# Optimization experiments

Measured on AMD Instinct MI355X. Metric: run time of the kernel, lower is better.

Reference implementation:

```python
import jax, jax.numpy as jnp
import numpy as np

EPS = 1e-6
NEG_SLOPE = 0.2

B, C_IN, N, K = 4, 64, 40960, 16
C_OUT = 64


def setup_inputs() -> dict:
    key = jax.random.key(0)
    k1, k2, k3 = jax.random.split(key, 3)
    feature = jax.random.normal(k1, (B, C_IN, N, 1), dtype=jnp.float32)
    neigh_idx = jax.random.randint(k2, (B, N, K), 0, N, dtype=jnp.int64)
    # 1x1 conv kernel [C_out, C_in] (kaiming-like scale), no bias since bn=True
    W = jax.random.normal(k3, (C_OUT, C_IN), dtype=jnp.float32) * np.float32(np.sqrt(2.0 / C_IN))
    gamma = jnp.ones((C_OUT,), dtype=jnp.float32)
    beta = jnp.zeros((C_OUT,), dtype=jnp.float32)
    return {"feature": feature, "W": W, "gamma": gamma, "beta": beta, "neigh_idx": neigh_idx}


def _gather_neighbour(pc, neigh_idx):
    # pc: [B, C, N]; neigh_idx: [B, N, K] -> [B, C, N, K]
    return jax.vmap(lambda p, idx: p[:, idx])(pc, neigh_idx)


def reference(feature, W, gamma, beta, neigh_idx):
    pc = feature[..., 0]                       # [B, C, N]
    f_neigh = _gather_neighbour(pc, neigh_idx) # [B, C, N, K]
    x = jnp.concatenate([feature, f_neigh], axis=-1)  # [B, C, N, K+1]
    # 1x1 conv (no bias)
    y = jnp.einsum('oc,bcnk->bonk', W, x)      # [B, C_out, N, K+1]
    # BatchNorm2d (training mode: batch stats over B,N,K+1), eps=1e-6
    mean = jnp.mean(y, axis=(0, 2, 3), keepdims=True)
    var = jnp.mean(jnp.square(y - mean), axis=(0, 2, 3), keepdims=True)
    yn = (y - mean) * jax.lax.rsqrt(var + EPS)
    yn = yn * gamma[None, :, None, None] + beta[None, :, None, None]
    # LeakyReLU(0.2)
    act = jnp.where(yn >= 0, yn, NEG_SLOPE * yn)
    # sum over neighbor axis, keepdim
    return jnp.sum(act, axis=-1, keepdims=True)  # [B, C_out, N, 1]
```

## Files before the change

kernel.cpp:

```cpp
#include <hip/hip_runtime.h>
#include <hip/hip_fp16.h>

typedef _Float16 h2 __attribute__((ext_vector_type(2)));
typedef _Float16 f16x8 __attribute__((ext_vector_type(8)));
typedef float f32x4 __attribute__((ext_vector_type(4)));
typedef unsigned int u32x4 __attribute__((ext_vector_type(4)));

#define BB 4
#define CIN 64
#define COUT 64
#define NN 40960
#define KK 16
#define GBLK (BB * NN / 256)
#define HP 32
#define HR 2
#define HBINS (NN / HR)
#define HWORDS (HBINS / 4)
#define GTP 72

__global__ __launch_bounds__(256) void k_hist(const int* __restrict__ idx,
                                              unsigned int* __restrict__ hist,
                                              float* __restrict__ sums) {
    __shared__ unsigned int bins[HWORDS];
    const int tid = threadIdx.x;
    const int p = blockIdx.x >> 3;
    const int b = (blockIdx.x & 7) >> 1;
    const int r = blockIdx.x & 1;
    const int lo = r * HBINS;

    if (blockIdx.x == 0 && tid < 128) sums[tid] = 0.f;

#pragma unroll
    for (int i = 0; i < HWORDS / 256; ++i) bins[i * 256 + tid] = 0u;
    __syncthreads();

    const int SHARE = NN * KK / HP;
    const int4* src = (const int4*)(idx + (size_t)b * NN * KK + (size_t)p * SHARE);
#pragma unroll 4
    for (int i = 0; i < SHARE / 4 / 256; ++i) {
        int4 v = src[i * 256 + tid];
        unsigned a0 = (unsigned)(v.x - lo), a1 = (unsigned)(v.y - lo);
        unsigned a2 = (unsigned)(v.z - lo), a3 = (unsigned)(v.w - lo);
        if (a0 < HBINS) atomicAdd(&bins[a0 >> 2], 1u << ((a0 & 3) * 8));
        if (a1 < HBINS) atomicAdd(&bins[a1 >> 2], 1u << ((a1 & 3) * 8));
        if (a2 < HBINS) atomicAdd(&bins[a2 >> 2], 1u << ((a2 & 3) * 8));
        if (a3 < HBINS) atomicAdd(&bins[a3 >> 2], 1u << ((a3 & 3) * 8));
    }
    __syncthreads();
    unsigned int* dst = hist + (size_t)((b * HP + p) * HR + r) * HWORDS;
#pragma unroll
    for (int i = 0; i < HWORDS / 256; ++i) dst[i * 256 + tid] = bins[i * 256 + tid];
}

__global__ __launch_bounds__(256) void k_gemm(const float* __restrict__ feat,
                                              const float* __restrict__ W,
                                              const unsigned int* __restrict__ hist,
                                              __half* __restrict__ g,
                                              float* __restrict__ sums) {
    __shared__ __half gt[4][64][GTP];
    __shared__ float  red[2][64][17];
    __shared__ float  w_s[256];

    const int tid   = threadIdx.x;
    const int b     = (blockIdx.x & 7) >> 1;
    const int chunk = (blockIdx.x & 1) * 80 + (blockIdx.x >> 3);
    const int n0    = chunk * 256;

    {
        const int n  = n0 + tid;
        const int r  = n / HBINS;
        const int ml = n - r * HBINS;
        const int w  = ml >> 2;
        const int sh = (ml & 3) * 8;
        unsigned s = 1u;
#pragma unroll
        for (int p = 0; p < HP; ++p)
            s += (hist[(size_t)((b * HP + p) * HR + r) * HWORDS + w] >> sh) & 0xffu;
        w_s[tid] = (float)s;
    }

    const int wv = tid >> 6;
    const int l  = tid & 63;
    const int lr = l & 15;
    const int lg = l >> 4;

    f16x8 bf[2][4];
#pragma unroll
    for (int ot = 0; ot < 4; ++ot)
#pragma unroll
        for (int kc = 0; kc < 2; ++kc) {
            const float* wp = W + (size_t)(ot * 16 + lr) * 64 + kc * 32 + lg * 8;
            float4 w0 = *(const float4*)(wp);
            float4 w1 = *(const float4*)(wp + 4);
            f16x8 t;
            t[0] = (_Float16)w0.x; t[1] = (_Float16)w0.y;
            t[2] = (_Float16)w0.z; t[3] = (_Float16)w0.w;
            t[4] = (_Float16)w1.x; t[5] = (_Float16)w1.y;
            t[6] = (_Float16)w1.z; t[7] = (_Float16)w1.w;
            bf[kc][ot] = t;
        }

    f32x4 acc[4][4];
#pragma unroll
    for (int i = 0; i < 4; ++i)
#pragma unroll
        for (int j = 0; j < 4; ++j) acc[i][j] = (f32x4)0.f;

    const float* fb = feat + (size_t)b * CIN * NN;
    const int nbase = n0 + wv * 64;

#pragma unroll
    for (int nt = 0; nt < 4; ++nt) {
        const int n = nbase + nt * 16 + lr;
#pragma unroll
        for (int kc = 0; kc < 2; ++kc) {
            const float* ap = fb + (size_t)(kc * 32 + lg * 8) * NN + n;
            f16x8 a;
#pragma unroll
            for (int j = 0; j < 8; ++j) a[j] = (_Float16)ap[(size_t)j * NN];
#pragma unroll
            for (int ot = 0; ot < 4; ++ot)
                acc[nt][ot] = __builtin_amdgcn_mfma_f32_16x16x32_f16(
                    a, bf[kc][ot], acc[nt][ot], 0, 0, 0);
        }
    }

    float wr[4][4];
#pragma unroll
    for (int nt = 0; nt < 4; ++nt)
#pragma unroll
        for (int r = 0; r < 4; ++r)
            wr[nt][r] = w_s[wv * 64 + nt * 16 + lg * 4 + r];

    float s1[4] = {0.f, 0.f, 0.f, 0.f}, s2[4] = {0.f, 0.f, 0.f, 0.f};
#pragma unroll
    for (int nt = 0; nt < 4; ++nt)
#pragma unroll
        for (int ot = 0; ot < 4; ++ot)
#pragma unroll
            for (int r = 0; r < 4; ++r) {
                float y = acc[nt][ot][r];
                float t = wr[nt][r] * y;
                s1[ot] += t;
                s2[ot] += t * y;
            }

#pragma unroll
    for (int nt = 0; nt < 4; ++nt)
#pragma unroll
        for (int ot = 0; ot < 4; ++ot)
#pragma unroll
            for (int r = 0; r < 4; ++r)
                gt[wv][nt * 16 + lg * 4 + r][ot * 16 + lr] = (__half)acc[nt][ot][r];

#pragma unroll
    for (int ot = 0; ot < 4; ++ot) {
        red[0][ot * 16 + lr][wv * 4 + lg] = s1[ot];
        red[1][ot * 16 + lr][wv * 4 + lg] = s2[ot];
    }
    __syncthreads();

    __half* gb = g + ((size_t)b * NN + n0) * 64;
#pragma unroll
    for (int i = 0; i < 8; ++i) {
        int nl = i * 32 + (tid >> 3);
        int o8 = (tid & 7) * 8;
        uint4 v = *(const uint4*)&gt[nl >> 6][nl & 63][o8];
        *(uint4*)&gb[(size_t)nl * 64 + o8] = v;
    }

    if (tid < 128) {
        int s = tid >> 6, o = tid & 63;
        float acc_s = 0.f;
#pragma unroll
        for (int t = 0; t < 16; ++t) acc_s += red[s][o][t];
        atomicAdd(&sums[s * 64 + o], acc_s);
    }
}

__global__ __launch_bounds__(256) void k_final(const __half* __restrict__ g,
                                               const int* __restrict__ idx,
                                               const float* __restrict__ sums,
                                               const float* __restrict__ gamma,
                                               const float* __restrict__ beta,
                                               float* __restrict__ out) {
    const int tid  = threadIdx.x;
    const int lane = tid & 63;
    const int wave = tid >> 6;
    const int b     = (blockIdx.x & 7) >> 1;
    const int chunk = ((blockIdx.x >> 3) << 1) | (blockIdx.x & 1);
    const int n0    = chunk * 64;

    __shared__ int   idx_s[64 * 17];
    __shared__ float tile[64 * 65];
    __shared__ float prm[128];

    {
        const u32x4* src = (const u32x4*)(idx + ((size_t)b * NN + n0) * KK);
        u32x4 v = __builtin_nontemporal_load(src + tid);
        int row = tid >> 2, col = (tid & 3) * 4;
        idx_s[row * 17 + col + 0] = (int)v.x;
        idx_s[row * 17 + col + 1] = (int)v.y;
        idx_s[row * 17 + col + 2] = (int)v.z;
        idx_s[row * 17 + col + 3] = (int)v.w;
    }

    if (tid < 64) {
        const double TOT = (double)BB * NN * (KK + 1);
        double mean = (double)sums[tid] / TOT;
        double var  = (double)sums[64 + tid] / TOT - mean * mean;
        double inv  = 1.0 / sqrt(var + 1e-6);
        float scale = (float)inv * gamma[tid];
        float shift = beta[tid] - (float)mean * scale;
        prm[tid]      = scale;
        prm[64 + tid] = shift;
    }
    __syncthreads();

    const int r  = lane >> 3;
    const int q8 = (lane & 7) * 8;
    h2 sc2[4], sh2[4];
#pragma unroll
    for (int h = 0; h < 4; ++h) {
        h2 a, s;
        a.x = (_Float16)prm[q8 + 2 * h];      a.y = (_Float16)prm[q8 + 2 * h + 1];
        s.x = (_Float16)prm[64 + q8 + 2 * h]; s.y = (_Float16)prm[64 + q8 + 2 * h + 1];
        sc2[h] = a; sh2[h] = s;
    }

    const __half* gb = g + (size_t)b * NN * 64;

#pragma unroll
    for (int rr = 0; rr < 2; ++rr) {
        const int nl = wave * 16 + rr * 8 + r;
        h2 acc[4];
#pragma unroll
        for (int h = 0; h < 4; ++h) acc[h] = (h2)(_Float16)0;

#pragma unroll
        for (int k = -1; k < KK; ++k) {
            int m = (k < 0) ? (n0 + nl) : idx_s[nl * 17 + k];
            union { uint4 u; h2 h[4]; } U;
            U.u = *(const uint4*)(gb + (size_t)m * 64 + q8);
#pragma unroll
            for (int h = 0; h < 4; ++h) {
                h2 t = U.h[h] * sc2[h] + sh2[h];
                acc[h] += __builtin_elementwise_max(t, t * (_Float16)0.2f);
            }
        }
        float* tr = &tile[nl * 65 + q8];
#pragma unroll
        for (int h = 0; h < 4; ++h) {
            tr[2 * h]     = (float)acc[h].x;
            tr[2 * h + 1] = (float)acc[h].y;
        }
    }
    __syncthreads();
    const int j   = tid & 63;
    const int sub = tid >> 6;
#pragma unroll
    for (int ob = 0; ob < 16; ++ob) {
        int o = ob * 4 + sub;
        __builtin_nontemporal_store(tile[j * 65 + o],
                                    &out[(size_t)(b * 64 + o) * NN + n0 + j]);
    }
}

extern "C" void kernel_launch(void* const* d_in, const int* in_sizes, int n_in,
                              void* d_out, int out_size, void* d_ws, size_t ws_size,
                              hipStream_t stream) {
    const float* feat  = (const float*)d_in[0];
    const float* W     = (const float*)d_in[1];
    const float* gamma = (const float*)d_in[2];
    const float* beta  = (const float*)d_in[3];
    const int*   idx   = (const int*)d_in[4];
    float* out = (float*)d_out;

    char* ws = (char*)d_ws;
    __half* g = (__half*)ws;
    size_t off = (size_t)BB * NN * 64 * sizeof(__half);
    unsigned int* hist = (unsigned int*)(ws + off);
    off += (size_t)BB * HP * HR * HWORDS * sizeof(unsigned int);
    float* sums = (float*)(ws + off);

    k_hist<<<BB * HP * HR, 256, 0, stream>>>(idx, hist, sums);
    k_gemm<<<GBLK, 256, 0, stream>>>(feat, W, hist, g, sums);
    k_final<<<(BB * NN) / 64, 256, 0, stream>>>(g, idx, sums, gamma, beta, out);
}
```

Before: 158.4 us.

## Swap MFMA operands to write g directly and reduce stats via shuffles

Measured after the change: 155.7 us, median of 2. Within noise of the previous version (-1.7%).

```diff
diff --git a/kernel.cpp b/kernel.cpp
--- a/kernel.cpp
+++ b/kernel.cpp
@@ -4,7 +4,6 @@
 typedef _Float16 h2 __attribute__((ext_vector_type(2)));
 typedef _Float16 f16x8 __attribute__((ext_vector_type(8)));
 typedef float f32x4 __attribute__((ext_vector_type(4)));
-typedef unsigned int u32x4 __attribute__((ext_vector_type(4)));
 
 #define BB 4
 #define CIN 64
@@ -16,7 +15,6 @@
 #define HR 2
 #define HBINS (NN / HR)
 #define HWORDS (HBINS / 4)
-#define GTP 72
 
 __global__ __launch_bounds__(256) void k_hist(const int* __restrict__ idx,
                                               unsigned int* __restrict__ hist,
@@ -57,9 +55,8 @@
                                               const unsigned int* __restrict__ hist,
                                               __half* __restrict__ g,
                                               float* __restrict__ sums) {
-    __shared__ __half gt[4][64][GTP];
-    __shared__ float  red[2][64][17];
-    __shared__ float  w_s[256];
+    __shared__ float red[2][64][5];
+    __shared__ float w_s[256];
 
     const int tid   = threadIdx.x;
     const int b     = (blockIdx.x & 7) >> 1;
@@ -84,7 +81,7 @@
     const int lr = l & 15;
     const int lg = l >> 4;
 
-    f16x8 bf[2][4];
+    f16x8 wf[2][4];
 #pragma unroll
     for (int ot = 0; ot < 4; ++ot)
 #pragma unroll
@@ -97,8 +94,9 @@
             t[2] = (_Float16)w0.z; t[3] = (_Float16)w0.w;
             t[4] = (_Float16)w1.x; t[5] = (_Float16)w1.y;
             t[6] = (_Float16)w1.z; t[7] = (_Float16)w1.w;
-            bf[kc][ot] = t;
-        }
+            wf[kc][ot] = t;
+        }
+    __syncthreads();
 
     f32x4 acc[4][4];
 #pragma unroll
@@ -112,69 +110,76 @@
 #pragma unroll
     for (int nt = 0; nt < 4; ++nt) {
         const int n = nbase + nt * 16 + lr;
+        f16x8 ff[2];
 #pragma unroll
         for (int kc = 0; kc < 2; ++kc) {
             const float* ap = fb + (size_t)(kc * 32 + lg * 8) * NN + n;
             f16x8 a;
 #pragma unroll
             for (int j = 0; j < 8; ++j) a[j] = (_Float16)ap[(size_t)j * NN];
-#pragma unroll
-            for (int ot = 0; ot < 4; ++ot)
+            ff[kc] = a;
+        }
+#pragma unroll
+        for (int ot = 0; ot < 4; ++ot)
+#pragma unroll
+            for (int kc = 0; kc < 2; ++kc)
                 acc[nt][ot] = __builtin_amdgcn_mfma_f32_16x16x32_f16(
-                    a, bf[kc][ot], acc[nt][ot], 0, 0, 0);
-        }
-    }
-
-    float wr[4][4];
-#pragma unroll
-    for (int nt = 0; nt < 4; ++nt)
-#pragma unroll
-        for (int r = 0; r < 4; ++r)
-            wr[nt][r] = w_s[wv * 64 + nt * 16 + lg * 4 + r];
-
-    float s1[4] = {0.f, 0.f, 0.f, 0.f}, s2[4] = {0.f, 0.f, 0.f, 0.f};
-#pragma unroll
-    for (int nt = 0; nt < 4; ++nt)
-#pragma unroll
-        for (int ot = 0; ot < 4; ++ot)
+                    wf[kc][ot], ff[kc], acc[nt][ot], 0, 0, 0);
+    }
+
+    __half* gb = g + ((size_t)b * NN + n0 + wv * 64) * 64;
+    float s1[4][4], s2[4][4];
+#pragma unroll
+    for (int ot = 0; ot < 4; ++ot)
+#pragma unroll
+        for (int r = 0; r < 4; ++r) { s1[ot][r] = 0.f; s2[ot][r] = 0.f; }
+
+#pragma unroll
+    for (int nt = 0; nt < 4; ++nt) {
+        const int nl = nt * 16 + lr;
+        const float w = w_s[wv * 64 + nl];
+#pragma unroll
+        for (int ot = 0; ot < 4; ++ot) {
+            union { uint2 u; h2 h[2]; } P;
+            h2 t0, t1;
+            t0.x = (_Float16)acc[nt][ot][0]; t0.y = (_Float16)acc[nt][ot][1];
+            t1.x = (_Float16)acc[nt][ot][2]; t1.y = (_Float16)acc[nt][ot][3];
+            P.h[0] = t0; P.h[1] = t1;
+            *(uint2*)&gb[(size_t)nl * 64 + ot * 16 + lg * 4] = P.u;
 #pragma unroll
             for (int r = 0; r < 4; ++r) {
                 float y = acc[nt][ot][r];
-                float t = wr[nt][r] * y;
-                s1[ot] += t;
-                s2[ot] += t * y;
-            }
-
-#pragma unroll
-    for (int nt = 0; nt < 4; ++nt)
+                float t = w * y;
+                s1[ot][r] += t;
+                s2[ot][r] += t * y;
+            }
+        }
+    }
+
+#pragma unroll
+    for (int m = 1; m < 16; m <<= 1)
 #pragma unroll
         for (int ot = 0; ot < 4; ++ot)
 #pragma unroll
-            for (int r = 0; r < 4; ++r)
-                gt[wv][nt * 16 + lg * 4 + r][ot * 16 + lr] = (__half)acc[nt][ot][r];
-
-#pragma unroll
-    for (int ot = 0; ot < 4; ++ot) {
-        red[0][ot * 16 + lr][wv * 4 + lg] = s1[ot];
-        red[1][ot * 16 + lr][wv * 4 + lg] = s2[ot];
-    }
-    __syncthreads();
-
-    __half* gb = g + ((size_t)b * NN + n0) * 64;
-#pragma unroll
-    for (int i = 0; i < 8; ++i) {
-        int nl = i * 32 + (tid >> 3);
-        int o8 = (tid & 7) * 8;
-        uint4 v = *(const uint4*)&gt[nl >> 6][nl & 63][o8];
-        *(uint4*)&gb[(size_t)nl * 64 + o8] = v;
-    }
-
+            for (int r = 0; r < 4; ++r) {
+                s1[ot][r] += __shfl_xor(s1[ot][r], m, 16);
+                s2[ot][r] += __shfl_xor(s2[ot][r], m, 16);
+            }
+
+    if (lr == 0) {
+#pragma unroll
+        for (int ot = 0; ot < 4; ++ot)
+#pragma unroll
+            for (int r = 0; r < 4; ++r) {
+                red[0][ot * 16 + lg * 4 + r][wv] = s1[ot][r];
+                red[1][ot * 16 + lg * 4 + r][wv] = s2[ot][r];
+            }
+    }
+    __syncthreads();
     if (tid < 128) {
-        int s = tid >> 6, o = tid & 63;
-        float acc_s = 0.f;
-#pragma unroll
-        for (int t = 0; t < 16; ++t) acc_s += red[s][o][t];
-        atomicAdd(&sums[s * 64 + o], acc_s);
+        int a = tid >> 6, o = tid & 63;
+        float s = (red[a][o][0] + red[a][o][1]) + (red[a][o][2] + red[a][o][3]);
+        atomicAdd(&sums[a * 64 + o], s);
     }
 }
 
@@ -196,13 +201,13 @@
     __shared__ float prm[128];
 
     {
-        const u32x4* src = (const u32x4*)(idx + ((size_t)b * NN + n0) * KK);
-        u32x4 v = __builtin_nontemporal_load(src + tid);
+        const int4* src = (const int4*)(idx + ((size_t)b * NN + n0) * KK);
+        int4 v = src[tid];
         int row = tid >> 2, col = (tid & 3) * 4;
-        idx_s[row * 17 + col + 0] = (int)v.x;
-        idx_s[row * 17 + col + 1] = (int)v.y;
-        idx_s[row * 17 + col + 2] = (int)v.z;
-        idx_s[row * 17 + col + 3] = (int)v.w;
+        idx_s[row * 17 + col + 0] = v.x;
+        idx_s[row * 17 + col + 1] = v.y;
+        idx_s[row * 17 + col + 2] = v.z;
+        idx_s[row * 17 + col + 3] = v.w;
     }
 
     if (tid < 64) {
@@ -261,8 +266,7 @@
 #pragma unroll
     for (int ob = 0; ob < 16; ++ob) {
         int o = ob * 4 + sub;
-        __builtin_nontemporal_store(tile[j * 65 + o],
-                                    &out[(size_t)(b * 64 + o) * NN + n0 + j]);
+        out[(size_t)(b * 64 + o) * NN + n0 + j] = tile[j * 65 + o];
     }
 }
 
```
